# Optimization experiments

Hardware: AMD Instinct MI355X
Metric: run time of the kernel (lower is better)

Reference implementation:

```python
import jax, jax.numpy as jnp
import numpy as np

N_NODES = 500_000
N_EDGES = 1_000_000
IN_DIM = 128
HID_DIM = 256
BN_EPS = 1e-5


def setup_inputs() -> dict:
    key = jax.random.key(0)
    ks = jax.random.split(key, 4)
    out = jax.random.normal(ks[0], (N_NODES, IN_DIM), dtype=jnp.float32)
    edge_label_index = jax.random.randint(ks[1], (2, N_EDGES), 0, N_NODES, dtype=jnp.int64)
    # Kaiming-uniform-ish init scale for linears
    W1 = jax.random.normal(ks[2], (IN_DIM, HID_DIM), dtype=jnp.float32) * (1.0 / np.sqrt(IN_DIM))
    b1 = jnp.zeros((HID_DIM,), dtype=jnp.float32)
    gamma = jnp.ones((HID_DIM,), dtype=jnp.float32)
    beta = jnp.zeros((HID_DIM,), dtype=jnp.float32)
    W2 = jax.random.normal(ks[3], (HID_DIM, 1), dtype=jnp.float32) * (1.0 / np.sqrt(HID_DIM))
    b2 = jnp.zeros((1,), dtype=jnp.float32)
    return {"out": out, "edge_label_index": edge_label_index,
            "W1": W1, "b1": b1, "gamma": gamma, "beta": beta, "W2": W2, "b2": b2}


def reference(out, edge_label_index, W1, b1, gamma, beta, W2, b2):
    src = edge_label_index[0]
    dst = edge_label_index[1]
    dot = out[src] * out[dst]                      # [E, IN_DIM] gather + hadamard
    h = dot @ W1 + b1                              # [E, HID_DIM]
    # BatchNorm1d (training mode: batch statistics, biased variance)
    mean = jnp.mean(h, axis=0)
    var = jnp.mean(jnp.square(h - mean), axis=0)
    h = (h - mean) * jax.lax.rsqrt(var + BN_EPS) * gamma + beta
    h = jax.nn.relu(h)
    y = h @ W2 + b2                                # [E, 1]
    return y.reshape(-1)
```

## Files before the change

kernel.cpp:

```cpp
#include <hip/hip_runtime.h>
#include <hip/hip_bf16.h>

#define N_NODES   500000
#define E_EDGES   1000000
#define TILE_E    32
#define N_TILES   (E_EDGES / TILE_E)
#define IN_DIM_K  128
#define HID_N     256
#define BN_EPS_F  1e-5f
#define MAIN_GRID 768
#define CONV_GRID 2048

typedef __attribute__((ext_vector_type(4))) float f32x4;
typedef __attribute__((ext_vector_type(2))) float f32x2;
typedef __attribute__((ext_vector_type(8))) short bf16x8;

__device__ __forceinline__ unsigned short f2bf(float f) {
    __hip_bfloat16 h = __float2bfloat16(f);
    return *reinterpret_cast<unsigned short*>(&h);
}
__device__ __forceinline__ unsigned pack2(float lo, float hi) {
    return (unsigned)f2bf(lo) | ((unsigned)f2bf(hi) << 16);
}
__device__ __forceinline__ unsigned bfmul2(unsigned a, unsigned b) {
    float alo = __uint_as_float(a << 16);
    float ahi = __uint_as_float(a & 0xffff0000u);
    float blo = __uint_as_float(b << 16);
    float bhi = __uint_as_float(b & 0xffff0000u);
    return pack2(alo * blo, ahi * bhi);
}
__device__ __forceinline__ void fp8mul4(unsigned ws, unsigned wd,
                                        unsigned& lo, unsigned& hi) {
    f32x2 s01 = __builtin_amdgcn_cvt_pk_f32_fp8(ws, false);
    f32x2 s23 = __builtin_amdgcn_cvt_pk_f32_fp8(ws, true);
    f32x2 d01 = __builtin_amdgcn_cvt_pk_f32_fp8(wd, false);
    f32x2 d23 = __builtin_amdgcn_cvt_pk_f32_fp8(wd, true);
    lo = pack2(s01[0] * d01[0], s01[1] * d01[1]);
    hi = pack2(s23[0] * d23[0], s23[1] * d23[1]);
}
__device__ __forceinline__ unsigned pk8(float4 a) {
    int r = __builtin_amdgcn_cvt_pk_fp8_f32(a.x, a.y, 0, false);
    r = __builtin_amdgcn_cvt_pk_fp8_f32(a.z, a.w, r, true);
    return (unsigned)r;
}

union FragU { uint4 u; bf16x8 v; unsigned w[4]; };

__global__ void zero_stats_kernel(float* g) {
    g[threadIdx.x] = 0.0f;
}

template <bool F8>
__global__ void convert_nodes_kernel(const float* __restrict__ in,
                                     unsigned* __restrict__ out16,
                                     unsigned* __restrict__ out8,
                                     float* __restrict__ gstat) {
    if (blockIdx.x == 0) {
        gstat[threadIdx.x] = 0.0f;
        gstat[256 + threadIdx.x] = 0.0f;
    }
    const size_t n4 = (size_t)N_NODES * IN_DIM_K / 8;
    size_t i = (size_t)blockIdx.x * blockDim.x + threadIdx.x;
    const size_t stride = (size_t)gridDim.x * blockDim.x;
    for (; i < n4; i += stride) {
        float4 a = reinterpret_cast<const float4*>(in)[2 * i];
        float4 b = reinterpret_cast<const float4*>(in)[2 * i + 1];
        uint4 o;
        o.x = pack2(a.x, a.y);
        o.y = pack2(a.z, a.w);
        o.z = pack2(b.x, b.y);
        o.w = pack2(b.z, b.w);
        reinterpret_cast<uint4*>(out16)[i] = o;
        if (F8) {
            uint2 p;
            p.x = pk8(a);
            p.y = pk8(b);
            reinterpret_cast<uint2*>(out8)[i] = p;
        }
    }
}

template <bool STATS, int MODE>
__global__ __launch_bounds__(256, 3)
void hadamard_mlp_kernel(const float* __restrict__ nodes,
                         const unsigned* __restrict__ nbf,
                         const unsigned* __restrict__ nf8,
                         const int* __restrict__ eidx,
                         const float* __restrict__ W1,
                         const float* __restrict__ W2,
                         const float* __restrict__ b2p,
                         float* __restrict__ gstat,
                         const float* __restrict__ gamma,
                         const float* __restrict__ beta,
                         float* __restrict__ y)
{
    __shared__ unsigned sh_d[2][TILE_E * 68];
    __shared__ float s_red[2][128];

    const int tid  = threadIdx.x;
    const int lane = tid & 63;
    const int wn   = tid >> 6;
    const int l15  = lane & 15;
    const int l4   = lane >> 4;

    bf16x8 bfrag[4][4];
    #pragma unroll
    for (int nt = 0; nt < 4; ++nt) {
        const int c = wn * 64 + nt * 16 + l15;
        #pragma unroll
        for (int kk = 0; kk < 4; ++kk) {
            const int kb = kk * 32 + 8 * l4;
            FragU t;
            #pragma unroll
            for (int j = 0; j < 4; ++j) {
                float w0 = W1[(kb + 2 * j    ) * HID_N + c];
                float w1 = W1[(kb + 2 * j + 1) * HID_N + c];
                t.w[j] = pack2(w0, w1);
            }
            bfrag[nt][kk] = t.v;
        }
    }

    float a_n[4], b_n[4], w2_n[4];
    if (!STATS) {
        const float inv_e = 1.0f / (float)E_EDGES;
        #pragma unroll
        for (int nt = 0; nt < 4; ++nt) {
            const int c = wn * 64 + nt * 16 + l15;
            float s  = gstat[c];
            float ss = gstat[256 + c];
            float mean = s * inv_e;
            float var  = fmaxf(ss * inv_e - mean * mean, 0.0f);
            float a = gamma[c] * rsqrtf(var + BN_EPS_F);
            a_n[nt]  = a;
            b_n[nt]  = beta[c] - mean * a;
            w2_n[nt] = W2[c];
        }
    }
    const float b2v = b2p[0];

    float s1[4] = {0.f, 0.f, 0.f, 0.f};
    float s2[4] = {0.f, 0.f, 0.f, 0.f};

    const int ge   = tid >> 3;
    const int part = tid & 7;

    uint4  ga[4];
    float4 hh[8];
    int si, di;

#define GATHER(SNODE, DNODE)                                                   \
    if constexpr (MODE == 2) {                                                 \
        ga[0] = *(reinterpret_cast<const uint4*>(nf8 + (size_t)(SNODE) * 32) + part); \
        ga[1] = *(reinterpret_cast<const uint4*>(nf8 + (size_t)(DNODE) * 32) + part); \
    } else if constexpr (MODE == 1) {                                          \
        const uint4* ps = reinterpret_cast<const uint4*>(nbf + (size_t)(SNODE) * 64) + part * 2; \
        const uint4* pd = reinterpret_cast<const uint4*>(nbf + (size_t)(DNODE) * 64) + part * 2; \
        ga[0] = ps[0]; ga[1] = ps[1]; ga[2] = pd[0]; ga[3] = pd[1];            \
    } else {                                                                   \
        const float4* ps = reinterpret_cast<const float4*>(nodes + (size_t)(SNODE) * IN_DIM_K) + part * 4; \
        const float4* pd = reinterpret_cast<const float4*>(nodes + (size_t)(DNODE) * IN_DIM_K) + part * 4; \
        _Pragma("unroll")                                                      \
        for (int j = 0; j < 4; ++j) { hh[j] = ps[j]; hh[4 + j] = pd[j]; }      \
    }

    const int t0 = blockIdx.x;
    {
        const int e0 = t0 * TILE_E + ge;
        const int s = eidx[e0];
        const int d = eidx[E_EDGES + e0];
        GATHER(s, d);
    }
    si = di = 0;
    if (t0 + MAIN_GRID < N_TILES) {
        const int e = (t0 + MAIN_GRID) * TILE_E + ge;
        si = eidx[e];  di = eidx[E_EDGES + e];
    }

    int cur = 0;
    int ptile = -1;

    for (int tile = t0; tile < N_TILES; tile += MAIN_GRID) {
        {
            unsigned buf[8];
            if constexpr (MODE == 2) {
                fp8mul4(ga[0].x, ga[1].x, buf[0], buf[1]);
                fp8mul4(ga[0].y, ga[1].y, buf[2], buf[3]);
                fp8mul4(ga[0].z, ga[1].z, buf[4], buf[5]);
                fp8mul4(ga[0].w, ga[1].w, buf[6], buf[7]);
            } else if constexpr (MODE == 1) {
                buf[0] = bfmul2(ga[0].x, ga[2].x); buf[1] = bfmul2(ga[0].y, ga[2].y);
                buf[2] = bfmul2(ga[0].z, ga[2].z); buf[3] = bfmul2(ga[0].w, ga[2].w);
                buf[4] = bfmul2(ga[1].x, ga[3].x); buf[5] = bfmul2(ga[1].y, ga[3].y);
                buf[6] = bfmul2(ga[1].z, ga[3].z); buf[7] = bfmul2(ga[1].w, ga[3].w);
            } else {
                #pragma unroll
                for (int j = 0; j < 4; ++j) {
                    buf[2*j]   = pack2(hh[j].x * hh[4+j].x, hh[j].y * hh[4+j].y);
                    buf[2*j+1] = pack2(hh[j].z * hh[4+j].z, hh[j].w * hh[4+j].w);
                }
            }
            unsigned* dst = sh_d[cur] + ge * 68 + part * 8;
            *reinterpret_cast<uint4*>(dst)     = *reinterpret_cast<const uint4*>(buf);
            *reinterpret_cast<uint4*>(dst + 4) = *reinterpret_cast<const uint4*>(buf + 4);
        }
        if (tile + MAIN_GRID < N_TILES) {
            GATHER(si, di);
        }
        if (tile + 2 * MAIN_GRID < N_TILES) {
            const int e = (tile + 2 * MAIN_GRID) * TILE_E + ge;
            si = eidx[e];  di = eidx[E_EDGES + e];
        }

        __syncthreads();

        if (!STATS && ptile >= 0 && tid < TILE_E) {
            const float* r = s_red[cur ^ 1];
            y[ptile * TILE_E + tid] = r[tid] + r[32 + tid] + r[64 + tid]
                                    + r[96 + tid] + b2v;
        }

        f32x4 acc[2][4] = {};
        __builtin_amdgcn_s_setprio(1);
        #pragma unroll
        for (int kk = 0; kk < 4; ++kk) {
            bf16x8 af[2];
            #pragma unroll
            for (int mt = 0; mt < 2; ++mt) {
                const int row = mt * 16 + l15;
                FragU t;
                t.u = *reinterpret_cast<const uint4*>(sh_d[cur] + row * 68 + kk * 16 + 4 * l4);
                af[mt] = t.v;
            }
            #pragma unroll
            for (int mt = 0; mt < 2; ++mt)
                #pragma unroll
                for (int nt = 0; nt < 4; ++nt)
                    acc[mt][nt] = __builtin_amdgcn_mfma_f32_16x16x32_bf16(
                        af[mt], bfrag[nt][kk], acc[mt][nt], 0, 0, 0);
        }
        __builtin_amdgcn_s_setprio(0);

        if (STATS) {
            #pragma unroll
            for (int nt = 0; nt < 4; ++nt) {
                float t1s = 0.f, t2s = 0.f;
                #pragma unroll
                for (int mt = 0; mt < 2; ++mt)
                    #pragma unroll
                    for (int r = 0; r < 4; ++r) {
                        float v = acc[mt][nt][r];
                        t1s += v;
                        t2s += v * v;
                    }
                s1[nt] += t1s;
                s2[nt] += t2s;
            }
        } else {
            float pw[2][4];
            #pragma unroll
            for (int mt = 0; mt < 2; ++mt)
                #pragma unroll
                for (int r = 0; r < 4; ++r) {
                    float acc_y = 0.f;
                    #pragma unroll
                    for (int nt = 0; nt < 4; ++nt) {
                        float z = acc[mt][nt][r] * a_n[nt] + b_n[nt];
                        z = fmaxf(z, 0.f);
                        acc_y += z * w2_n[nt];
                    }
                    pw[mt][r] = acc_y;
                }
            #pragma unroll
            for (int off = 1; off < 16; off <<= 1)
                #pragma unroll
                for (int mt = 0; mt < 2; ++mt)
                    #pragma unroll
                    for (int r = 0; r < 4; ++r)
                        pw[mt][r] += __shfl_xor(pw[mt][r], off, 64);
            if (l15 == 0) {
                #pragma unroll
                for (int mt = 0; mt < 2; ++mt)
                    #pragma unroll
                    for (int r = 0; r < 4; ++r) {
                        const int el = mt * 16 + l4 * 4 + r;
                        s_red[cur][wn * 32 + el] = pw[mt][r];
                    }
            }
            ptile = tile;
        }
        cur ^= 1;
    }
#undef GATHER

    if (STATS) {
        #pragma unroll
        for (int nt = 0; nt < 4; ++nt) {
            s1[nt] += __shfl_xor(s1[nt], 16, 64);
            s1[nt] += __shfl_xor(s1[nt], 32, 64);
            s2[nt] += __shfl_xor(s2[nt], 16, 64);
            s2[nt] += __shfl_xor(s2[nt], 32, 64);
        }
        if (l4 == 0) {
            #pragma unroll
            for (int nt = 0; nt < 4; ++nt) {
                const int c = wn * 64 + nt * 16 + l15;
                atomicAdd(&gstat[c],       s1[nt]);
                atomicAdd(&gstat[256 + c], s2[nt]);
            }
        }
    } else {
        __syncthreads();
        if (ptile >= 0 && tid < TILE_E) {
            const float* r = s_red[cur ^ 1];
            y[ptile * TILE_E + tid] = r[tid] + r[32 + tid] + r[64 + tid]
                                    + r[96 + tid] + b2v;
        }
    }
}

extern "C" void kernel_launch(void* const* d_in, const int* in_sizes, int n_in,
                              void* d_out, int out_size, void* d_ws, size_t ws_size,
                              hipStream_t stream) {
    const float* nodes = (const float*)d_in[0];
    const int*   eidx  = (const int*)d_in[1];
    const float* W1    = (const float*)d_in[2];
    const float* gamma = (const float*)d_in[4];
    const float* beta  = (const float*)d_in[5];
    const float* W2    = (const float*)d_in[6];
    const float* b2    = (const float*)d_in[7];

    float* ws    = (float*)d_ws;
    float* gstat = ws;
    const size_t BF_BYTES = (size_t)N_NODES * IN_DIM_K * 2;
    const size_t F8_BYTES = (size_t)N_NODES * IN_DIM_K;
    unsigned* nbf = (unsigned*)((char*)d_ws + 4096);
    unsigned* nf8 = (unsigned*)((char*)d_ws + 4096 + BF_BYTES);
    float* y     = (float*)d_out;

    const bool lvl2 = ws_size >= 4096 + BF_BYTES + F8_BYTES;
    const bool lvl1 = ws_size >= 4096 + BF_BYTES;

    if (lvl2) {
        convert_nodes_kernel<true><<<CONV_GRID, 256, 0, stream>>>(nodes, nbf, nf8, gstat);
        hadamard_mlp_kernel<true, 2><<<MAIN_GRID, 256, 0, stream>>>(
            nodes, nbf, nf8, eidx, W1, W2, b2, gstat, gamma, beta, y);
        hadamard_mlp_kernel<false, 1><<<MAIN_GRID, 256, 0, stream>>>(
            nodes, nbf, nf8, eidx, W1, W2, b2, gstat, gamma, beta, y);
    } else if (lvl1) {
        convert_nodes_kernel<false><<<CONV_GRID, 256, 0, stream>>>(nodes, nbf, nf8, gstat);
        hadamard_mlp_kernel<true, 1><<<MAIN_GRID, 256, 0, stream>>>(
            nodes, nbf, nf8, eidx, W1, W2, b2, gstat, gamma, beta, y);
        hadamard_mlp_kernel<false, 1><<<MAIN_GRID, 256, 0, stream>>>(
            nodes, nbf, nf8, eidx, W1, W2, b2, gstat, gamma, beta, y);
    } else {
        zero_stats_kernel<<<1, 512, 0, stream>>>(gstat);
        hadamard_mlp_kernel<true, 0><<<MAIN_GRID, 256, 0, stream>>>(
            nodes, nbf, nf8, eidx, W1, W2, b2, gstat, gamma, beta, y);
        hadamard_mlp_kernel<false, 0><<<MAIN_GRID, 256, 0, stream>>>(
            nodes, nbf, nf8, eidx, W1, W2, b2, gstat, gamma, beta, y);
    }
}
```

Baseline: 266.5 us.

## Add dedicated stats kernel with W1 held in LDS and per-wave 16-edge tiles

Replaces the stats pass of the shared hadamard-MLP template with a dedicated kernel. Each block transposes W1 to bf16 once into LDS, and each wave independently processes 16-edge tiles from fp8 node features, double-buffering gathers across two tiles. Per-wave register accumulators feed MFMA-computed column sums and squared sums, which are reduced through LDS atomics and then global atomics. This is meant to remove the per-tile block barriers and shared-memory staging of the old stats pass and to raise gather parallelism. In exchange it uses more LDS (about 70KB per block) and register pressure, which limits occupancy.

```diff
diff --git a/kernel.cpp b/kernel.cpp
--- a/kernel.cpp
+++ b/kernel.cpp
@@ -5,10 +5,12 @@
 #define E_EDGES   1000000
 #define TILE_E    32
 #define N_TILES   (E_EDGES / TILE_E)
+#define NWT       62500
 #define IN_DIM_K  128
 #define HID_N     256
 #define BN_EPS_F  1e-5f
 #define MAIN_GRID 768
+#define P1_GRID   512
 #define CONV_GRID 2048
 
 typedef __attribute__((ext_vector_type(4))) float f32x4;
@@ -80,11 +82,132 @@
     }
 }
 
+__global__ __launch_bounds__(256, 2)
+void stats_mfree_kernel(const unsigned* __restrict__ nf8,
+                        const int* __restrict__ eidx,
+                        const float* __restrict__ W1,
+                        float* __restrict__ gstat)
+{
+    __shared__ unsigned short w1t[256][136];
+    __shared__ float s_red[512];
+
+    const int tid  = threadIdx.x;
+    const int lane = tid & 63;
+    const int w    = tid >> 6;
+    const int l15  = lane & 15;
+    const int l4   = lane >> 4;
+
+    {
+        const int c = tid;
+        #pragma unroll 8
+        for (int k = 0; k < IN_DIM_K; ++k)
+            w1t[c][k] = f2bf(W1[k * HID_N + c]);
+        s_red[tid] = 0.f;
+        s_red[256 + tid] = 0.f;
+    }
+    __syncthreads();
+
+    float s1[16], s2[16];
+    #pragma unroll
+    for (int i = 0; i < 16; ++i) { s1[i] = 0.f; s2[i] = 0.f; }
+
+    const int W    = gridDim.x * 4;
+    const int wsid = blockIdx.x * 4 + w;
+
+    uint2 sa[4], da[4], sb[4], db[4];
+    int siA, diA, siB, diB;
+
+#define P1_GATHER(SA, DA, SN, DN)                                              \
+    {   const uint2* ps = reinterpret_cast<const uint2*>(nf8 + (size_t)(SN) * 32) + l4; \
+        const uint2* pd = reinterpret_cast<const uint2*>(nf8 + (size_t)(DN) * 32) + l4; \
+        _Pragma("unroll")                                                      \
+        for (int kk = 0; kk < 4; ++kk) { SA[kk] = ps[kk * 4]; DA[kk] = pd[kk * 4]; } }
+
+    {
+        int t = wsid;
+        if (t < NWT) {
+            const int s = eidx[t * 16 + l15];
+            const int d = eidx[E_EDGES + t * 16 + l15];
+            P1_GATHER(sa, da, s, d);
+        }
+        t = wsid + W;
+        if (t < NWT) {
+            const int s = eidx[t * 16 + l15];
+            const int d = eidx[E_EDGES + t * 16 + l15];
+            P1_GATHER(sb, db, s, d);
+        }
+    }
+    siA = diA = siB = diB = 0;
+    if (wsid + 2 * W < NWT) {
+        siA = eidx[(wsid + 2 * W) * 16 + l15];
+        diA = eidx[E_EDGES + (wsid + 2 * W) * 16 + l15];
+    }
+    if (wsid + 3 * W < NWT) {
+        siB = eidx[(wsid + 3 * W) * 16 + l15];
+        diB = eidx[E_EDGES + (wsid + 3 * W) * 16 + l15];
+    }
+
+#define P1_BODY(T, SA, DA, SIV, DIV)                                           \
+    {                                                                          \
+        bf16x8 af[4];                                                          \
+        _Pragma("unroll")                                                      \
+        for (int kk = 0; kk < 4; ++kk) {                                       \
+            FragU t_;                                                          \
+            fp8mul4(SA[kk].x, DA[kk].x, t_.w[0], t_.w[1]);                     \
+            fp8mul4(SA[kk].y, DA[kk].y, t_.w[2], t_.w[3]);                     \
+            af[kk] = t_.v;                                                     \
+        }                                                                      \
+        if ((T) + 2 * W < NWT) { P1_GATHER(SA, DA, SIV, DIV); }                \
+        if ((T) + 4 * W < NWT) {                                               \
+            SIV = eidx[((T) + 4 * W) * 16 + l15];                              \
+            DIV = eidx[E_EDGES + ((T) + 4 * W) * 16 + l15];                    \
+        }                                                                      \
+        _Pragma("unroll")                                                      \
+        for (int nt = 0; nt < 16; ++nt) {                                      \
+            f32x4 acc = {0.f, 0.f, 0.f, 0.f};                                  \
+            _Pragma("unroll")                                                  \
+            for (int kk = 0; kk < 4; ++kk) {                                   \
+                FragU b_;                                                      \
+                b_.u = *reinterpret_cast<const uint4*>(&w1t[nt * 16 + l15][kk * 32 + l4 * 8]); \
+                acc = __builtin_amdgcn_mfma_f32_16x16x32_bf16(af[kk], b_.v, acc, 0, 0, 0); \
+            }                                                                  \
+            const float v0 = acc[0], v1 = acc[1], v2 = acc[2], v3 = acc[3];    \
+            s1[nt] += (v0 + v1) + (v2 + v3);                                   \
+            s2[nt] += (v0 * v0 + v1 * v1) + (v2 * v2 + v3 * v3);               \
+        }                                                                      \
+    }
+
+    for (int t = wsid; t < NWT; t += 2 * W) {
+        P1_BODY(t, sa, da, siA, diA);
+        const int tb = t + W;
+        if (tb < NWT) { P1_BODY(tb, sb, db, siB, diB); }
+    }
+#undef P1_BODY
+#undef P1_GATHER
+
+    #pragma unroll
+    for (int nt = 0; nt < 16; ++nt) {
+        s1[nt] += __shfl_xor(s1[nt], 16, 64);
+        s1[nt] += __shfl_xor(s1[nt], 32, 64);
+        s2[nt] += __shfl_xor(s2[nt], 16, 64);
+        s2[nt] += __shfl_xor(s2[nt], 32, 64);
+    }
+    if (l4 == 0) {
+        #pragma unroll
+        for (int nt = 0; nt < 16; ++nt) {
+            atomicAdd(&s_red[nt * 16 + l15],       s1[nt]);
+            atomicAdd(&s_red[256 + nt * 16 + l15], s2[nt]);
+        }
+    }
+    __syncthreads();
+    atomicAdd(&gstat[tid],       s_red[tid]);
+    atomicAdd(&gstat[256 + tid], s_red[256 + tid]);
+}
+
 template <bool STATS, int MODE>
 __global__ __launch_bounds__(256, 3)
 void hadamard_mlp_kernel(const float* __restrict__ nodes,
                          const unsigned* __restrict__ nbf,
-                         const unsigned* __restrict__ nf8,
                          const int* __restrict__ eidx,
                          const float* __restrict__ W1,
                          const float* __restrict__ W2,
@@ -144,16 +267,14 @@
 
     const int ge   = tid >> 3;
     const int part = tid & 7;
+    const int G = gridDim.x;
 
     uint4  ga[4];
-    float4 hh[8];
+    float4 ha[8];
     int si, di;
 
 #define GATHER(SNODE, DNODE)                                                   \
-    if constexpr (MODE == 2) {                                                 \
-        ga[0] = *(reinterpret_cast<const uint4*>(nf8 + (size_t)(SNODE) * 32) + part); \
-        ga[1] = *(reinterpret_cast<const uint4*>(nf8 + (size_t)(DNODE) * 32) + part); \
-    } else if constexpr (MODE == 1) {                                          \
+    if constexpr (MODE == 1) {                                                 \
         const uint4* ps = reinterpret_cast<const uint4*>(nbf + (size_t)(SNODE) * 64) + part * 2; \
         const uint4* pd = reinterpret_cast<const uint4*>(nbf + (size_t)(DNODE) * 64) + part * 2; \
         ga[0] = ps[0]; ga[1] = ps[1]; ga[2] = pd[0]; ga[3] = pd[1];            \
@@ -161,7 +282,7 @@
         const float4* ps = reinterpret_cast<const float4*>(nodes + (size_t)(SNODE) * IN_DIM_K) + part * 4; \
         const float4* pd = reinterpret_cast<const float4*>(nodes + (size_t)(DNODE) * IN_DIM_K) + part * 4; \
         _Pragma("unroll")                                                      \
-        for (int j = 0; j < 4; ++j) { hh[j] = ps[j]; hh[4 + j] = pd[j]; }      \
+        for (int j = 0; j < 4; ++j) { ha[j] = ps[j]; ha[4 + j] = pd[j]; }      \
     }
 
     const int t0 = blockIdx.x;
@@ -172,23 +293,18 @@
         GATHER(s, d);
     }
     si = di = 0;
-    if (t0 + MAIN_GRID < N_TILES) {
-        const int e = (t0 + MAIN_GRID) * TILE_E + ge;
+    if (t0 + G < N_TILES) {
+        const int e = (t0 + G) * TILE_E + ge;
         si = eidx[e];  di = eidx[E_EDGES + e];
     }
 
     int cur = 0;
     int ptile = -1;
 
-    for (int tile = t0; tile < N_TILES; tile += MAIN_GRID) {
+    for (int tile = t0; tile < N_TILES; tile += G) {
         {
             unsigned buf[8];
-            if constexpr (MODE == 2) {
-                fp8mul4(ga[0].x, ga[1].x, buf[0], buf[1]);
-                fp8mul4(ga[0].y, ga[1].y, buf[2], buf[3]);
-                fp8mul4(ga[0].z, ga[1].z, buf[4], buf[5]);
-                fp8mul4(ga[0].w, ga[1].w, buf[6], buf[7]);
-            } else if constexpr (MODE == 1) {
+            if constexpr (MODE == 1) {
                 buf[0] = bfmul2(ga[0].x, ga[2].x); buf[1] = bfmul2(ga[0].y, ga[2].y);
                 buf[2] = bfmul2(ga[0].z, ga[2].z); buf[3] = bfmul2(ga[0].w, ga[2].w);
                 buf[4] = bfmul2(ga[1].x, ga[3].x); buf[5] = bfmul2(ga[1].y, ga[3].y);
@@ -196,19 +312,19 @@
             } else {
                 #pragma unroll
                 for (int j = 0; j < 4; ++j) {
-                    buf[2*j]   = pack2(hh[j].x * hh[4+j].x, hh[j].y * hh[4+j].y);
-                    buf[2*j+1] = pack2(hh[j].z * hh[4+j].z, hh[j].w * hh[4+j].w);
+                    buf[2*j]   = pack2(ha[j].x * ha[4+j].x, ha[j].y * ha[4+j].y);
+                    buf[2*j+1] = pack2(ha[j].z * ha[4+j].z, ha[j].w * ha[4+j].w);
                 }
             }
             unsigned* dst = sh_d[cur] + ge * 68 + part * 8;
             *reinterpret_cast<uint4*>(dst)     = *reinterpret_cast<const uint4*>(buf);
             *reinterpret_cast<uint4*>(dst + 4) = *reinterpret_cast<const uint4*>(buf + 4);
         }
-        if (tile + MAIN_GRID < N_TILES) {
+        if (tile + G < N_TILES) {
             GATHER(si, di);
         }
-        if (tile + 2 * MAIN_GRID < N_TILES) {
-            const int e = (tile + 2 * MAIN_GRID) * TILE_E + ge;
+        if (tile + 2 * G < N_TILES) {
+            const int e = (tile + 2 * G) * TILE_E + ge;
             si = eidx[e];  di = eidx[E_EDGES + e];
         }
 
@@ -343,21 +459,20 @@
 
     if (lvl2) {
         convert_nodes_kernel<true><<<CONV_GRID, 256, 0, stream>>>(nodes, nbf, nf8, gstat);
-        hadamard_mlp_kernel<true, 2><<<MAIN_GRID, 256, 0, stream>>>(
-            nodes, nbf, nf8, eidx, W1, W2, b2, gstat, gamma, beta, y);
+        stats_mfree_kernel<<<P1_GRID, 256, 0, stream>>>(nf8, eidx, W1, gstat);
         hadamard_mlp_kernel<false, 1><<<MAIN_GRID, 256, 0, stream>>>(
-            nodes, nbf, nf8, eidx, W1, W2, b2, gstat, gamma, beta, y);
+            nodes, nbf, eidx, W1, W2, b2, gstat, gamma, beta, y);
     } else if (lvl1) {
         convert_nodes_kernel<false><<<CONV_GRID, 256, 0, stream>>>(nodes, nbf, nf8, gstat);
         hadamard_mlp_kernel<true, 1><<<MAIN_GRID, 256, 0, stream>>>(
-            nodes, nbf, nf8, eidx, W1, W2, b2, gstat, gamma, beta, y);
+            nodes, nbf, eidx, W1, W2, b2, gstat, gamma, beta, y);
         hadamard_mlp_kernel<false, 1><<<MAIN_GRID, 256, 0, stream>>>(
-            nodes, nbf, nf8, eidx, W1, W2, b2, gstat, gamma, beta, y);
+            nodes, nbf, eidx, W1, W2, b2, gstat, gamma, beta, y);
     } else {
         zero_stats_kernel<<<1, 512, 0, stream>>>(gstat);
         hadamard_mlp_kernel<true, 0><<<MAIN_GRID, 256, 0, stream>>>(
-            nodes, nbf, nf8, eidx, W1, W2, b2, gstat, gamma, beta, y);
+            nodes, nbf, eidx, W1, W2, b2, gstat, gamma, beta, y);
         hadamard_mlp_kernel<false, 0><<<MAIN_GRID, 256, 0, stream>>>(
-            nodes, nbf, nf8, eidx, W1, W2, b2, gstat, gamma, beta, y);
-    }
-}
+            nodes, nbf, eidx, W1, W2, b2, gstat, gamma, beta, y);
+    }
+}
```

Result: slower. 448.6 us (+68.4%).
